# Performance work log

Measured on AMD Instinct MI355X. Metric: run time of the kernel, lower is better.

Reference implementation:

```python
import jax, jax.numpy as jnp
import numpy as np
import math


def _rope_2d(k, height, width):
    """Additive 2D sinusoidal position embedding. k: (B, N, D), N == height*width."""
    B, N, D = k.shape
    d_half = D // 2
    y_idx = jnp.arange(height, dtype=jnp.float32) / max(height - 1, 1)
    x_idx = jnp.arange(width, dtype=jnp.float32) / max(width - 1, 1)
    y_grid, x_grid = jnp.meshgrid(y_idx, x_idx, indexing='ij')
    y_flat = y_grid.reshape(-1)  # (N,)
    x_flat = x_grid.reshape(-1)
    freq = jnp.exp(jnp.arange(0, d_half, 2, dtype=jnp.float32) * (-(math.log(10000.0) / d_half)))

    def pos_half(flat, scale):
        ang = flat[:, None] * freq[None, :] * scale  # (N, ceil(d_half/2))
        p = jnp.zeros((N, d_half), dtype=jnp.float32)
        p = p.at[:, 0::2].set(jnp.sin(ang))
        n_odd = p[:, 1::2].shape[-1]
        p = p.at[:, 1::2].set(jnp.cos(ang[:, :n_odd]))
        return p

    pos_emb = jnp.concatenate([pos_half(y_flat, float(height)), pos_half(x_flat, float(width))], axis=-1)
    if pos_emb.shape[-1] < D:
        pos_emb = jnp.pad(pos_emb, ((0, 0), (0, D - pos_emb.shape[-1])))
    elif pos_emb.shape[-1] > D:
        pos_emb = pos_emb[:, :D]
    return k + pos_emb[None]


def setup_inputs() -> dict:
    key = jax.random.key(0)
    k1, k2, k3, k4 = jax.random.split(key, 4)
    B, N, dim = 2, 4096, 768
    num_heads, key_dim = 2, 8
    # xavier-uniform-like scales
    sq = math.sqrt(6.0 / (dim + num_heads * (key_dim + 1)))
    sk = math.sqrt(6.0 / (dim + key_dim))
    return {
        'query_tokens': jax.random.normal(k1, (B, N, dim), dtype=jnp.float32),
        'key_tokens': jax.random.normal(k2, (B, N, dim), dtype=jnp.float32),
        'Wq': jax.random.uniform(k3, (dim, num_heads * (key_dim + 1)), minval=-sq, maxval=sq, dtype=jnp.float32),
        'Wk': jax.random.uniform(k4, (dim, key_dim), minval=-sk, maxval=sk, dtype=jnp.float32),
        'spatial_bias': jnp.zeros((1, 1, 1), dtype=jnp.float32),
        'height': 64,
        'width': 64,
    }


def reference(query_tokens, key_tokens, Wq, Wk, spatial_bias, height, width):
    key_dim = Wk.shape[-1]
    num_heads = Wq.shape[-1] // (key_dim + 1)
    scale = key_dim ** (-0.5)
    B, N_q, _ = query_tokens.shape
    qw = (query_tokens @ Wq).reshape(B, N_q, num_heads, key_dim + 1)
    q = qw[..., :key_dim]          # (B, Nq, H, d)
    w = qw[..., -1]                # (B, Nq, H)
    k = key_tokens @ Wk            # (B, Nk, d)
    if height is not None and width is not None:
        k = _rope_2d(k, height, width)
    scores = jax.nn.relu(jnp.einsum('bqhd,bkd->bhqk', q, k) * scale)  # (B,H,Nq,Nk)
    index_scores = jnp.einsum('bqh,bhqk->bqk', w, scores)
    return index_scores + spatial_bias
```

## Files before the change

kernel.cpp:

```cpp
#include <hip/hip_runtime.h>
#include <math.h>

#define BB 2
#define NN 4096
#define DIM 768
#define QSTRIDE 20
#define SCALE 0.35355339059327373f

__global__ __launch_bounds__(256) void proj_kernel(const float* __restrict__ qt,
                                                   const float* __restrict__ kt,
                                                   const float* __restrict__ Wq,
                                                   const float* __restrict__ Wk,
                                                   const int* __restrict__ hp,
                                                   const int* __restrict__ wp,
                                                   float* __restrict__ qd,
                                                   float* __restrict__ kd) {
  __shared__ float lw[DIM * 18];

  const int tid = threadIdx.x;
  const int lane = tid & 63;
  const int r = lane >> 5;
  const int l = lane & 31;

  if (blockIdx.x < 512) {
    {
      const float4* s4 = (const float4*)Wq;
      float4* d4 = (float4*)lw;
#pragma unroll 1
      for (int t = tid; t < DIM * 18 / 4; t += 256) d4[t] = s4[t];
    }
    __syncthreads();

    const int row0 = (blockIdx.x * 4 + (tid >> 6)) * 4;
    const float* xr = qt + (size_t)row0 * DIM;

    float acc[4][18];
#pragma unroll
    for (int rr = 0; rr < 4; ++rr)
#pragma unroll
      for (int c = 0; c < 18; ++c) acc[rr][c] = 0.f;

#pragma unroll
    for (int j = 0; j < DIM / 64; ++j) {
      const int i = lane + 64 * j;
      const float x0 = xr[i];
      const float x1 = xr[i + DIM];
      const float x2 = xr[i + 2 * DIM];
      const float x3 = xr[i + 3 * DIM];
      const float* wr = lw + i * 18;
#pragma unroll
      for (int c = 0; c < 9; ++c) {
        const float2 w2 = *(const float2*)(wr + 2 * c);
        acc[0][2*c] = fmaf(x0, w2.x, acc[0][2*c]);
        acc[0][2*c+1] = fmaf(x0, w2.y, acc[0][2*c+1]);
        acc[1][2*c] = fmaf(x1, w2.x, acc[1][2*c]);
        acc[1][2*c+1] = fmaf(x1, w2.y, acc[1][2*c+1]);
        acc[2][2*c] = fmaf(x2, w2.x, acc[2][2*c]);
        acc[2][2*c+1] = fmaf(x2, w2.y, acc[2][2*c+1]);
        acc[3][2*c] = fmaf(x3, w2.x, acc[3][2*c]);
        acc[3][2*c+1] = fmaf(x3, w2.y, acc[3][2*c+1]);
      }
    }

#pragma unroll
    for (int off = 32; off >= 1; off >>= 1)
#pragma unroll
      for (int rr = 0; rr < 4; ++rr)
#pragma unroll
        for (int c = 0; c < 18; ++c)
          acc[rr][c] += __shfl_xor(acc[rr][c], off, 64);

    if (l < 18) {
      int src;
      if (l < 8) src = l;
      else if (l < 16) src = l + 1;
      else if (l == 16) src = 8;
      else src = 17;
      float v0 = 0.f, v1 = 0.f;
#pragma unroll
      for (int c = 0; c < 18; ++c) {
        const float a0 = r ? acc[1][c] : acc[0][c];
        const float a1 = r ? acc[3][c] : acc[2][c];
        v0 = (src == c) ? a0 : v0;
        v1 = (src == c) ? a1 : v1;
      }
      if (l >= 16) { v0 *= SCALE; v1 *= SCALE; }
      qd[(size_t)(row0 + r) * QSTRIDE + l] = v0;
      qd[(size_t)(row0 + 2 + r) * QSTRIDE + l] = v1;
    }
  } else {
    const int pair = (blockIdx.x - 512) * 4 + (tid >> 6);
    const int row0 = pair * 2;
    const float* xr0 = kt + (size_t)row0 * DIM;
    const float* xr1 = xr0 + DIM;

    float acc0[8], acc1[8];
#pragma unroll
    for (int c = 0; c < 8; ++c) { acc0[c] = 0.f; acc1[c] = 0.f; }

#pragma unroll
    for (int j = 0; j < DIM / 64; ++j) {
      const int i = lane + 64 * j;
      const float x0 = xr0[i];
      const float x1 = xr1[i];
      const float4 wa = *(const float4*)(Wk + i * 8);
      const float4 wb = *(const float4*)(Wk + i * 8 + 4);
      acc0[0] = fmaf(x0, wa.x, acc0[0]); acc0[1] = fmaf(x0, wa.y, acc0[1]);
      acc0[2] = fmaf(x0, wa.z, acc0[2]); acc0[3] = fmaf(x0, wa.w, acc0[3]);
      acc0[4] = fmaf(x0, wb.x, acc0[4]); acc0[5] = fmaf(x0, wb.y, acc0[5]);
      acc0[6] = fmaf(x0, wb.z, acc0[6]); acc0[7] = fmaf(x0, wb.w, acc0[7]);
      acc1[0] = fmaf(x1, wa.x, acc1[0]); acc1[1] = fmaf(x1, wa.y, acc1[1]);
      acc1[2] = fmaf(x1, wa.z, acc1[2]); acc1[3] = fmaf(x1, wa.w, acc1[3]);
      acc1[4] = fmaf(x1, wb.x, acc1[4]); acc1[5] = fmaf(x1, wb.y, acc1[5]);
      acc1[6] = fmaf(x1, wb.z, acc1[6]); acc1[7] = fmaf(x1, wb.w, acc1[7]);
    }

#pragma unroll
    for (int off = 32; off >= 1; off >>= 1)
#pragma unroll
      for (int c = 0; c < 8; ++c) {
        acc0[c] += __shfl_xor(acc0[c], off, 64);
        acc1[c] += __shfl_xor(acc1[c], off, 64);
      }

    if (l < 8) {
      const int row = row0 + r;
      const int h = hp[0];
      const int w = wp[0];
      const int n = row % NN;
      const int yi = n / w;
      const int xi = n - yi * w;
      const int hd = (h - 1) > 1 ? (h - 1) : 1;
      const int wd = (w - 1) > 1 ? (w - 1) : 1;
      const float yv = (float)yi / (float)hd;
      const float xv = (float)xi / (float)wd;
      const float base = (l < 4) ? yv : xv;
      const float sc = (l < 4) ? (float)h : (float)w;
      const float fr = (l & 2) ? 0.01f : 1.0f;
      const float ang = base * fr * sc;
      const float pe = (l & 1) ? cosf(ang) : sinf(ang);
      float v = r ? acc1[0] : acc0[0];
#pragma unroll
      for (int c = 1; c < 8; ++c) {
        const float cand = r ? acc1[c] : acc0[c];
        v = (l == c) ? cand : v;
      }
      kd[(size_t)row * 8 + l] = v + pe;
    }
  }
}

__global__ __launch_bounds__(256) void scores_kernel(const float* __restrict__ qd,
                                                     const float* __restrict__ kd,
                                                     const float* __restrict__ bias,
                                                     float* __restrict__ out) {
  const int lane = threadIdx.x & 63;
  const int wv = __builtin_amdgcn_readfirstlane(threadIdx.x >> 6);
  const int kb = blockIdx.x;
  const int qb = blockIdx.y;
  const int b  = blockIdx.z;

  const float* kp = kd + ((size_t)b * NN + kb * 64 + lane) * 8;
  const float4 k0 = *(const float4*)kp;
  const float4 k1 = *(const float4*)(kp + 4);
  const float sb = bias[0];

  const int row0 = qb * 32 + wv * 8;
  const float* qp = qd + ((size_t)b * NN + row0) * QSTRIDE;
  float* op = out + ((size_t)b * NN + row0) * (size_t)NN + (size_t)(kb * 64 + lane);

#pragma unroll
  for (int rr = 0; rr < 8; ++rr) {
    const float* q = qp + rr * QSTRIDE;
    float d0 = q[0] * k0.x;
    d0 = fmaf(q[1], k0.y, d0);
    d0 = fmaf(q[2], k0.z, d0);
    d0 = fmaf(q[3], k0.w, d0);
    d0 = fmaf(q[4], k1.x, d0);
    d0 = fmaf(q[5], k1.y, d0);
    d0 = fmaf(q[6], k1.z, d0);
    d0 = fmaf(q[7], k1.w, d0);
    float d1 = q[8] * k0.x;
    d1 = fmaf(q[9],  k0.y, d1);
    d1 = fmaf(q[10], k0.z, d1);
    d1 = fmaf(q[11], k0.w, d1);
    d1 = fmaf(q[12], k1.x, d1);
    d1 = fmaf(q[13], k1.y, d1);
    d1 = fmaf(q[14], k1.z, d1);
    d1 = fmaf(q[15], k1.w, d1);
    d0 = fmaxf(d0, 0.f);
    d1 = fmaxf(d1, 0.f);
    op[(size_t)rr * NN] = fmaf(q[16], d0, fmaf(q[17], d1, sb));
  }
}

extern "C" void kernel_launch(void* const* d_in, const int* in_sizes, int n_in,
                              void* d_out, int out_size, void* d_ws, size_t ws_size,
                              hipStream_t stream) {
  const float* qt = (const float*)d_in[0];
  const float* kt = (const float*)d_in[1];
  const float* Wq = (const float*)d_in[2];
  const float* Wk = (const float*)d_in[3];
  const float* sb = (const float*)d_in[4];
  const int* hp = (const int*)d_in[5];
  const int* wp = (const int*)d_in[6];

  float* qd = (float*)d_ws;
  float* kd = qd + (size_t)BB * NN * QSTRIDE;
  float* outp = (float*)d_out;

  proj_kernel<<<1536, 256, 0, stream>>>(qt, kt, Wq, Wk, hp, wp, qd, kd);
  scores_kernel<<<dim3(64, NN / 32, BB), 256, 0, stream>>>(qd, kd, sb, outp);
}
```

Baseline: 204.7 us.

## Remap projection so each lane owns one output element, dropping shuffle reductions

```diff
diff --git a/kernel.cpp b/kernel.cpp
--- a/kernel.cpp
+++ b/kernel.cpp
@@ -3,9 +3,11 @@
 
 #define BB 2
 #define NN 4096
+#define TOT (BB * NN)
 #define DIM 768
 #define QSTRIDE 20
 #define SCALE 0.35355339059327373f
+#define QBLOCKS 683
 
 __global__ __launch_bounds__(256) void proj_kernel(const float* __restrict__ qt,
                                                    const float* __restrict__ kt,
@@ -15,138 +17,76 @@
                                                    const int* __restrict__ wp,
                                                    float* __restrict__ qd,
                                                    float* __restrict__ kd) {
-  __shared__ float lw[DIM * 18];
-
   const int tid = threadIdx.x;
   const int lane = tid & 63;
-  const int r = lane >> 5;
-  const int l = lane & 31;
+  const int wv = tid >> 6;
 
-  if (blockIdx.x < 512) {
-    {
-      const float4* s4 = (const float4*)Wq;
-      float4* d4 = (float4*)lw;
-#pragma unroll 1
-      for (int t = tid; t < DIM * 18 / 4; t += 256) d4[t] = s4[t];
+  if (blockIdx.x < QBLOCKS) {
+    const int r = lane / 18;
+    const int c = lane - r * 18;
+    const int row = (blockIdx.x * 4 + wv) * 3 + r;
+    const bool valid = (r < 3) && (row < TOT);
+    const float* xr = qt + (size_t)(valid ? row : 0) * DIM;
+    const float* wc = Wq + c;
+
+    float a0 = 0.f, a1 = 0.f, a2 = 0.f, a3 = 0.f;
+#pragma unroll 4
+    for (int k4 = 0; k4 < DIM / 4; ++k4) {
+      const float4 xv = *(const float4*)(xr + k4 * 4);
+      const float w0 = wc[(k4 * 4 + 0) * 18];
+      const float w1 = wc[(k4 * 4 + 1) * 18];
+      const float w2 = wc[(k4 * 4 + 2) * 18];
+      const float w3 = wc[(k4 * 4 + 3) * 18];
+      a0 = fmaf(xv.x, w0, a0);
+      a1 = fmaf(xv.y, w1, a1);
+      a2 = fmaf(xv.z, w2, a2);
+      a3 = fmaf(xv.w, w3, a3);
     }
-    __syncthreads();
+    float v = (a0 + a1) + (a2 + a3);
 
-    const int row0 = (blockIdx.x * 4 + (tid >> 6)) * 4;
-    const float* xr = qt + (size_t)row0 * DIM;
+    int slot;
+    if (c < 8) slot = c;
+    else if (c == 8) slot = 16;
+    else if (c == 17) slot = 17;
+    else slot = c - 1;
+    if (c == 8 || c == 17) v *= SCALE;
+    if (valid) qd[(size_t)row * QSTRIDE + slot] = v;
+  } else {
+    const int r = lane >> 3;
+    const int c = lane & 7;
+    const int row = ((blockIdx.x - QBLOCKS) * 4 + wv) * 8 + r;
+    const float* xr = kt + (size_t)row * DIM;
+    const float* wc = Wk + c;
 
-    float acc[4][18];
-#pragma unroll
-    for (int rr = 0; rr < 4; ++rr)
-#pragma unroll
-      for (int c = 0; c < 18; ++c) acc[rr][c] = 0.f;
+    float a0 = 0.f, a1 = 0.f, a2 = 0.f, a3 = 0.f;
+#pragma unroll 4
+    for (int k4 = 0; k4 < DIM / 4; ++k4) {
+      const float4 xv = *(const float4*)(xr + k4 * 4);
+      const float w0 = wc[(k4 * 4 + 0) * 8];
+      const float w1 = wc[(k4 * 4 + 1) * 8];
+      const float w2 = wc[(k4 * 4 + 2) * 8];
+      const float w3 = wc[(k4 * 4 + 3) * 8];
+      a0 = fmaf(xv.x, w0, a0);
+      a1 = fmaf(xv.y, w1, a1);
+      a2 = fmaf(xv.z, w2, a2);
+      a3 = fmaf(xv.w, w3, a3);
+    }
+    float v = (a0 + a1) + (a2 + a3);
 
-#pragma unroll
-    for (int j = 0; j < DIM / 64; ++j) {
-      const int i = lane + 64 * j;
-      const float x0 = xr[i];
-      const float x1 = xr[i + DIM];
-      const float x2 = xr[i + 2 * DIM];
-      const float x3 = xr[i + 3 * DIM];
-      const float* wr = lw + i * 18;
-#pragma unroll
-      for (int c = 0; c < 9; ++c) {
-        const float2 w2 = *(const float2*)(wr + 2 * c);
-        acc[0][2*c] = fmaf(x0, w2.x, acc[0][2*c]);
-        acc[0][2*c+1] = fmaf(x0, w2.y, acc[0][2*c+1]);
-        acc[1][2*c] = fmaf(x1, w2.x, acc[1][2*c]);
-        acc[1][2*c+1] = fmaf(x1, w2.y, acc[1][2*c+1]);
-        acc[2][2*c] = fmaf(x2, w2.x, acc[2][2*c]);
-        acc[2][2*c+1] = fmaf(x2, w2.y, acc[2][2*c+1]);
-        acc[3][2*c] = fmaf(x3, w2.x, acc[3][2*c]);
-        acc[3][2*c+1] = fmaf(x3, w2.y, acc[3][2*c+1]);
-      }
-    }
+    const int h = hp[0];
+    const int w = wp[0];
+    const int n = row & (NN - 1);
+    const int yi = n / w;
+    const int xi = n - yi * w;
+    const int hd = (h - 1) > 1 ? (h - 1) : 1;
+    const int wd = (w - 1) > 1 ? (w - 1) : 1;
+    const float base = (c < 4) ? ((float)yi / (float)hd) : ((float)xi / (float)wd);
+    const float sc = (c < 4) ? (float)h : (float)w;
+    const float fr = (c & 2) ? 0.01f : 1.0f;
+    const float ang = base * fr * sc;
+    const float pe = (c & 1) ? cosf(ang) : sinf(ang);
 
-#pragma unroll
-    for (int off = 32; off >= 1; off >>= 1)
-#pragma unroll
-      for (int rr = 0; rr < 4; ++rr)
-#pragma unroll
-        for (int c = 0; c < 18; ++c)
-          acc[rr][c] += __shfl_xor(acc[rr][c], off, 64);
-
-    if (l < 18) {
-      int src;
-      if (l < 8) src = l;
-      else if (l < 16) src = l + 1;
-      else if (l == 16) src = 8;
-      else src = 17;
-      float v0 = 0.f, v1 = 0.f;
-#pragma unroll
-      for (int c = 0; c < 18; ++c) {
-        const float a0 = r ? acc[1][c] : acc[0][c];
-        const float a1 = r ? acc[3][c] : acc[2][c];
-        v0 = (src == c) ? a0 : v0;
-        v1 = (src == c) ? a1 : v1;
-      }
-      if (l >= 16) { v0 *= SCALE; v1 *= SCALE; }
-      qd[(size_t)(row0 + r) * QSTRIDE + l] = v0;
-      qd[(size_t)(row0 + 2 + r) * QSTRIDE + l] = v1;
-    }
-  } else {
-    const int pair = (blockIdx.x - 512) * 4 + (tid >> 6);
-    const int row0 = pair * 2;
-    const float* xr0 = kt + (size_t)row0 * DIM;
-    const float* xr1 = xr0 + DIM;
-
-    float acc0[8], acc1[8];
-#pragma unroll
-    for (int c = 0; c < 8; ++c) { acc0[c] = 0.f; acc1[c] = 0.f; }
-
-#pragma unroll
-    for (int j = 0; j < DIM / 64; ++j) {
-      const int i = lane + 64 * j;
-      const float x0 = xr0[i];
-      const float x1 = xr1[i];
-      const float4 wa = *(const float4*)(Wk + i * 8);
-      const float4 wb = *(const float4*)(Wk + i * 8 + 4);
-      acc0[0] = fmaf(x0, wa.x, acc0[0]); acc0[1] = fmaf(x0, wa.y, acc0[1]);
-      acc0[2] = fmaf(x0, wa.z, acc0[2]); acc0[3] = fmaf(x0, wa.w, acc0[3]);
-      acc0[4] = fmaf(x0, wb.x, acc0[4]); acc0[5] = fmaf(x0, wb.y, acc0[5]);
-      acc0[6] = fmaf(x0, wb.z, acc0[6]); acc0[7] = fmaf(x0, wb.w, acc0[7]);
-      acc1[0] = fmaf(x1, wa.x, acc1[0]); acc1[1] = fmaf(x1, wa.y, acc1[1]);
-      acc1[2] = fmaf(x1, wa.z, acc1[2]); acc1[3] = fmaf(x1, wa.w, acc1[3]);
-      acc1[4] = fmaf(x1, wb.x, acc1[4]); acc1[5] = fmaf(x1, wb.y, acc1[5]);
-      acc1[6] = fmaf(x1, wb.z, acc1[6]); acc1[7] = fmaf(x1, wb.w, acc1[7]);
-    }
-
-#pragma unroll
-    for (int off = 32; off >= 1; off >>= 1)
-#pragma unroll
-      for (int c = 0; c < 8; ++c) {
-        acc0[c] += __shfl_xor(acc0[c], off, 64);
-        acc1[c] += __shfl_xor(acc1[c], off, 64);
-      }
-
-    if (l < 8) {
-      const int row = row0 + r;
-      const int h = hp[0];
-      const int w = wp[0];
-      const int n = row % NN;
-      const int yi = n / w;
-      const int xi = n - yi * w;
-      const int hd = (h - 1) > 1 ? (h - 1) : 1;
-      const int wd = (w - 1) > 1 ? (w - 1) : 1;
-      const float yv = (float)yi / (float)hd;
-      const float xv = (float)xi / (float)wd;
-      const float base = (l < 4) ? yv : xv;
-      const float sc = (l < 4) ? (float)h : (float)w;
-      const float fr = (l & 2) ? 0.01f : 1.0f;
-      const float ang = base * fr * sc;
-      const float pe = (l & 1) ? cosf(ang) : sinf(ang);
-      float v = r ? acc1[0] : acc0[0];
-#pragma unroll
-      for (int c = 1; c < 8; ++c) {
-        const float cand = r ? acc1[c] : acc0[c];
-        v = (l == c) ? cand : v;
-      }
-      kd[(size_t)row * 8 + l] = v + pe;
-    }
+    kd[(size_t)row * 8 + c] = v + pe;
   }
 }
 
@@ -206,9 +146,9 @@
   const int* wp = (const int*)d_in[6];
 
   float* qd = (float*)d_ws;
-  float* kd = qd + (size_t)BB * NN * QSTRIDE;
+  float* kd = qd + (size_t)TOT * QSTRIDE;
   float* outp = (float*)d_out;
 
-  proj_kernel<<<1536, 256, 0, stream>>>(qt, kt, Wq, Wk, hp, wp, qd, kd);
+  proj_kernel<<<QBLOCKS + 256, 256, 0, stream>>>(qt, kt, Wq, Wk, hp, wp, qd, kd);
   scores_kernel<<<dim3(64, NN / 32, BB), 256, 0, stream>>>(qd, kd, sb, outp);
 }
```

New measurement: 260.8 us. 1.27x slower.
